# Optimization experiments

Measured on AMD Instinct MI355X. Metric: run time of the kernel, lower is better.

## Reference

```python
import jax, jax.numpy as jnp
import numpy as np

H, L, N = 512, 4096, 64

def make_dplr_hippo(n):
    # HiPPO-LegS -> NPLR -> DPLR diagonalization (numpy, init-time only)
    p0 = np.sqrt(1 + 2 * np.arange(n))
    A = p0[:, None] * p0[None, :]
    A = -(np.tril(A) - np.diag(np.arange(n)))
    p = np.sqrt(np.arange(n) + 0.5)
    b = np.sqrt(2 * np.arange(n) + 1.0)
    S = A + p[:, None] * p[None, :]
    Lambda_re = np.full(n, np.diagonal(S).mean())
    Lambda_im, V = np.linalg.eigh(S * -1j)
    Pc = V.conj().T @ p
    Bc = V.conj().T @ b
    return Lambda_re, Lambda_im, Pc, Bc

def setup_inputs() -> dict:
    key = jax.random.key(0)
    k_u, k_c, k_s = jax.random.split(key, 3)
    lr, li, Pc, Bc = make_dplr_hippo(N)
    tile = lambda v: jnp.tile(jnp.asarray(v, jnp.float32)[None, :], (H, 1))
    dt_min, dt_max = 0.001, 0.1
    log_step = (jax.random.uniform(k_s, (H, 1), jnp.float32)
                * (np.log(dt_max) - np.log(dt_min)) + np.log(dt_min))
    return {
        "u": jax.random.normal(k_u, (H, L), jnp.float32),
        "Lambda_re": tile(lr), "Lambda_im": tile(li),
        "P_re": tile(Pc.real), "P_im": tile(Pc.imag),
        "B_re": tile(Bc.real), "B_im": tile(Bc.imag),
        "C": jax.random.normal(k_c, (H, N, 2), jnp.float32) * (0.5 ** 0.5),
        "D": jnp.ones((H, 1), jnp.float32),
        "log_step": log_step,
    }

def reference(u, Lambda_re, Lambda_im, P_re, P_im, B_re, B_im, C, D, log_step):
    # u: [H, L]; all params leading dim H (vmapped channels)
    Lam = jnp.minimum(Lambda_re, -1e-4) + 1j * Lambda_im      # [H, N]
    P = P_re + 1j * P_im                                       # [H, N]
    B = B_re + 1j * B_im                                       # [H, N]
    Cc = C[..., 0] + 1j * C[..., 1]                             # [H, N]
    step = jnp.exp(log_step)                                    # [H, 1]
    Lseq = u.shape[-1]
    Omega = jnp.exp(-2j * jnp.pi * (jnp.arange(Lseq) / Lseq)).astype(jnp.complex64)  # [L]
    g = (2.0 / step) * ((1.0 - Omega) / (1.0 + Omega))[None, :]  # [H, L]
    c = 2.0 / (1.0 + Omega)                                      # [L]
    denom = 1.0 / (g[:, :, None] - Lam[:, None, :])              # [H, L, N]
    cauchy = lambda v: jnp.einsum('hn,hln->hl', v, denom)
    k00 = cauchy(Cc.conj() * B)
    k01 = cauchy(Cc.conj() * P)
    k10 = cauchy(P.conj() * B)
    k11 = cauchy(P.conj() * P)
    atRoots = c[None, :] * (k00 - k01 * (1.0 / (1.0 + k11)) * k10)
    K = jnp.fft.ifft(atRoots, Lseq, axis=-1).real                # [H, L] conv kernel
    # causal convolution via zero-padded FFT (length 2L)
    ud = jnp.fft.rfft(u, n=2 * Lseq, axis=-1)
    Kd = jnp.fft.rfft(K, n=2 * Lseq, axis=-1)
    y = jnp.fft.irfft(ud * Kd, n=2 * Lseq, axis=-1)[..., :Lseq]
    return y + D * u
```

## Files before the change

### kernel.cpp

```cpp
#include <hip/hip_runtime.h>
#include <math.h>

#define NT 512

typedef float v2 __attribute__((ext_vector_type(2)));

__device__ __forceinline__ v2 vrot(v2 a){ return (v2){-a.y, a.x}; }
__device__ __forceinline__ v2 vconj(v2 a){ return (v2){a.x, -a.y}; }
__device__ __forceinline__ v2 vcmul(v2 a, v2 b){ return a.x*b + a.y*vrot(b); }
__device__ __forceinline__ v2 vcmulc(v2 a, v2 b){
    return a.x*(v2){b.x, -b.y} + a.y*(v2){b.y, b.x};
}
__device__ __forceinline__ v2 vfma1(float s, v2 v, v2 acc){
    return (v2){ __builtin_fmaf(s, v.x, acc.x), __builtin_fmaf(s, v.y, acc.y) };
}

__device__ __forceinline__ int SW(int e){ return e ^ (((e>>5) ^ (e>>9)) & 15); }

__device__ __forceinline__ int d8r4(int x){
    return ((x&7)<<9) | (((x>>3)&7)<<6) | (((x>>6)&7)<<3) | ((x>>9)&7);
}
__device__ __forceinline__ int rev3(int t){
    return ((t&7)<<6) | (t&56) | ((t>>6)&7);
}

__device__ __forceinline__ void load_row(const v2* twd, int rowIdx, v2 W[7]) {
    const float4* rp4 = (const float4*)(twd + rowIdx*8);
    float4 q0 = rp4[0], q1 = rp4[1], q2 = rp4[2], q3 = rp4[3];
    W[0]=(v2){q0.x,q0.y}; W[1]=(v2){q0.z,q0.w}; W[2]=(v2){q1.x,q1.y};
    W[3]=(v2){q1.z,q1.w}; W[4]=(v2){q2.x,q2.y}; W[5]=(v2){q2.z,q2.w};
    W[6]=(v2){q3.x,q3.y};
}

__device__ __forceinline__ void dft8_inv(v2 t[8], v2 y[8]) {
    const float RH = 0.70710678f;
    v2 p  = t[0]+t[4], m  = t[0]-t[4], q  = t[2]+t[6], r  = t[2]-t[6];
    v2 rr = vrot(r);
    v2 E0 = p+q, E2 = p-q, E1 = m+rr, E3 = m-rr;
    v2 p2 = t[1]+t[5], m2 = t[1]-t[5], q2 = t[3]+t[7], r2 = t[3]-t[7];
    v2 rr2 = vrot(r2);
    v2 O0 = p2+q2, O2 = p2-q2, O1 = m2+rr2, O3 = m2-rr2;
    v2 W1O = RH*(O1 + vrot(O1));
    v2 W2O = vrot(O2);
    v2 W3O = vrot(RH*(O3 + vrot(O3)));
    y[0] = E0 + O0;  y[4] = E0 - O0;
    y[1] = E1 + W1O; y[5] = E1 - W1O;
    y[2] = E2 + W2O; y[6] = E2 - W2O;
    y[3] = E3 + W3O; y[7] = E3 - W3O;
}

__device__ __forceinline__ void dft8_inv_lo4(v2 t[8], v2 y[4]) {
    const float RH = 0.70710678f;
    v2 p  = t[0]+t[4], m  = t[0]-t[4], q  = t[2]+t[6], r  = t[2]-t[6];
    v2 rr = vrot(r);
    v2 E0 = p+q, E2 = p-q, E1 = m+rr, E3 = m-rr;
    v2 p2 = t[1]+t[5], m2 = t[1]-t[5], q2 = t[3]+t[7], r2 = t[3]-t[7];
    v2 rr2 = vrot(r2);
    v2 O0 = p2+q2, O2 = p2-q2, O1 = m2+rr2, O3 = m2-rr2;
    v2 W1O = RH*(O1 + vrot(O1));
    v2 W2O = vrot(O2);
    v2 W3O = vrot(RH*(O3 + vrot(O3)));
    y[0] = E0 + O0;
    y[1] = E1 + W1O;
    y[2] = E2 + W2O;
    y[3] = E3 + W3O;
}

__device__ __forceinline__ void dft8_fwd(v2 t[8], v2 y[8]) {
    const float RH = 0.70710678f;
    v2 p  = t[0]+t[4], m  = t[0]-t[4], q  = t[2]+t[6], r  = t[2]-t[6];
    v2 rr = vrot(r);
    v2 E0 = p+q, E2 = p-q, E1 = m-rr, E3 = m+rr;
    v2 p2 = t[1]+t[5], m2 = t[1]-t[5], q2 = t[3]+t[7], r2 = t[3]-t[7];
    v2 rr2 = vrot(r2);
    v2 O0 = p2+q2, O2 = p2-q2, O1 = m2-rr2, O3 = m2+rr2;
    v2 W1O = RH*(O1 - vrot(O1));
    v2 W2O = (v2){O2.y, -O2.x};
    v2 W3O = (-RH)*(O3 + vrot(O3));
    y[0] = E0 + O0;  y[4] = E0 - O0;
    y[1] = E1 + W1O; y[5] = E1 - W1O;
    y[2] = E2 + W2O; y[6] = E2 - W2O;
    y[3] = E3 + W3O; y[7] = E3 - W3O;
}


template<int Q, bool BAR>
__device__ __forceinline__ void r8_dit_inv(v2* buf, int tid, const v2* twd) {
    int j = tid & (Q-1);
    v2 W[7];
    load_row(twd, (512/Q)*j, W);
    int base = 8*tid - 7*j;
    v2 t[8];
    #pragma unroll
    for (int k = 0; k < 8; ++k) t[k] = buf[SW(base + k*Q)];
    #pragma unroll
    for (int k = 0; k < 7; ++k) t[k+1] = vcmul(t[k+1], W[k]);
    v2 y[8];
    dft8_inv(t, y);
    #pragma unroll
    for (int m = 0; m < 8; ++m) buf[SW(base + m*Q)] = y[m];
    if (BAR) __syncthreads();
    else     __builtin_amdgcn_wave_barrier();
}

template<int Q, bool BAR>
__device__ __forceinline__ void r8_dif_fwd(v2* buf, int tid, const v2* twd) {
    int j = tid & (Q-1);
    int baseL = 8*tid - 7*j;
    v2 W[7];
    if (Q > 1) load_row(twd, (512/Q)*j, W);
    #pragma unroll 1
    for (int hh = 0; hh < 2; ++hh) {
        int base = baseL + (hh << 12);
        v2 t[8];
        #pragma unroll
        for (int k = 0; k < 8; ++k) t[k] = buf[SW(base + k*Q)];
        v2 y[8];
        dft8_fwd(t, y);
        if (Q > 1) {
            #pragma unroll
            for (int k = 0; k < 7; ++k) y[k+1] = vcmulc(y[k+1], W[k]);
        }
        #pragma unroll
        for (int m = 0; m < 8; ++m) buf[SW(base + m*Q)] = y[m];
    }
    if (BAR) __syncthreads();
    else     __builtin_amdgcn_wave_barrier();
}

__global__ void __launch_bounds__(64)
s4_prep(const float* __restrict__ Lre, const float* __restrict__ Lim,
        const float* __restrict__ Pre, const float* __restrict__ Pim,
        const float* __restrict__ Bre, const float* __restrict__ Bim,
        const float* __restrict__ Cin,
        float* __restrict__ ws8, float* __restrict__ ws1)
{
    int idx = blockIdx.x*64 + threadIdx.x;
    float lre = fminf(Lre[idx], -1e-4f);
    float lim = Lim[idx];
    float pr = Pre[idx], pi = Pim[idx];
    float br = Bre[idx], bi = Bim[idx];
    float cr = Cin[2*idx], ci = Cin[2*idx+1];
    v2 cc = (v2){cr, -ci};
    v2 w00 = vcmul(cc, (v2){br, bi});
    v2 w01 = vcmul(cc, (v2){pr, pi});
    v2 w10 = vcmul((v2){pr,-pi}, (v2){br, bi});
    float* o = ws8 + idx*8;
    o[0] = -lre;  o[1] = -lim;
    o[2] = w00.x; o[3] = w00.y;
    o[4] = w01.x; o[5] = w01.y;
    o[6] = w10.x; o[7] = w10.y;
    ws1[idx] = pr*pr + pi*pi;
}

__global__ void __launch_bounds__(NT)
s4_twprep(v2* __restrict__ twd)
{
    int j = threadIdx.x;
    const float fm = 6.2831853072f / 4096.0f;
    #pragma unroll
    for (int k = 0; k < 7; ++k) {
        float s, c; __sincosf(fm * (float)(j*(k+1)), &s, &c);
        twd[j*8 + k] = (v2){c, s};
    }
    twd[j*8 + 7] = (v2){1.0f, 0.0f};
}

__global__ void __launch_bounds__(NT)
s4_fused(const float* __restrict__ u,
         const float* __restrict__ Din, const float* __restrict__ logstep,
         const float* __restrict__ ws8, const float* __restrict__ ws1,
         const v2* __restrict__ twd,
         float* __restrict__ out)
{
    __shared__ v2 buf[8192];
    const int tid = threadIdx.x;
    const int h = blockIdx.x;

    const float step = expf(logstep[h]);
    const float tos  = 2.0f / step;
    const float hstep = 0.5f * step;
    const float* pp = ws8 + (h*64)*8;
    const float* pw = ws1 + h*64;

    v2 a4[4];
    #pragma unroll 1
    for (int hp = 0; hp < 2; ++hp) {
        float tv[4];
        v2 cf[4], k00[4], k01[4], k10[4], k11[4];
        const int lbase = hp*(4*NT);
        #pragma unroll
        for (int i = 0; i < 4; ++i) {
            int l = lbase + i*NT + tid;
            float ang = -6.2831855f * ((float)l * (1.0f/4096.0f));
            float sh, ch; __sincosf(0.5f*ang, &sh, &ch);
            float traw = -tos * sh * __builtin_amdgcn_rcpf(ch);
            float t = fminf(fmaxf(traw, -1e18f), 1e18f);
            tv[i] = t;
            cf[i] = (v2){1.0f, t*hstep};
            k00[i]=(v2)(0.0f); k01[i]=(v2)(0.0f); k10[i]=(v2)(0.0f); k11[i]=(v2)(0.0f);
        }
        #pragma unroll 4
        for (int n = 0; n < 64; ++n) {
            float nlre = pp[n*8+0], nlim = pp[n*8+1];
            v2 w00 = (v2){pp[n*8+2], pp[n*8+3]};
            v2 w01 = (v2){pp[n*8+4], pp[n*8+5]};
            v2 w10 = (v2){pp[n*8+6], pp[n*8+7]};
            float w11r = pw[n];
            float lre2 = nlre*nlre;
            #pragma unroll
            for (int i = 0; i < 4; ++i) {
                float s = tv[i] + nlim;
                float inv = __builtin_amdgcn_rcpf(__builtin_fmaf(s, s, lre2));
                v2 p = (v2){nlre, s} * inv;
                v2 cp = (v2){p.x, -p.y};
                v2 rp = (v2){p.y,  p.x};
                k00[i] = vfma1(w00.y, rp, vfma1(w00.x, cp, k00[i]));
                k01[i] = vfma1(w01.y, rp, vfma1(w01.x, cp, k01[i]));
                k10[i] = vfma1(w10.y, rp, vfma1(w10.x, cp, k10[i]));
                k11[i] = vfma1(w11r,  cp, k11[i]);
            }
        }
        #pragma unroll
        for (int i = 0; i < 4; ++i) {
            v2 opk = (v2){1.0f + k11[i].x, k11[i].y};
            float iv = __builtin_amdgcn_rcpf(opk.x*opk.x + opk.y*opk.y);
            v2 r11 = vconj(opk) * iv;
            v2 t  = vcmul(vcmul(k01[i], r11), k10[i]);
            v2 res = vcmul(cf[i], k00[i] - t);
            if (hp == 0) buf[SW(tid + 512*i)] = res;
            else         a4[i] = res;
        }
    }
    {
        v2 t[8];
        #pragma unroll
        for (int k = 0; k < 4; ++k) t[k] = buf[SW(tid + 512*k)];
        #pragma unroll
        for (int k = 0; k < 4; ++k) t[4+k] = a4[k];
        __syncthreads();
        v2 y[8];
        dft8_inv(t, y);
        int tb8 = 8*rev3(tid);
        #pragma unroll
        for (int m = 0; m < 8; ++m) buf[SW(tb8 + m)] = y[m];
    }
    __syncthreads();

    r8_dit_inv<8,  false>(buf, tid, twd);
    r8_dit_inv<64, true >(buf, tid, twd);

    {
        v2 W[7];
        load_row(twd, tid, W);
        v2 t[8];
        #pragma unroll
        for (int k = 0; k < 8; ++k) t[k] = buf[SW(tid + 512*k)];
        #pragma unroll
        for (int k = 0; k < 7; ++k) t[k+1] = vcmul(t[k+1], W[k]);
        v2 y[8];
        dft8_inv(t, y);
        float uval[8];
        const float* up = u + h*4096;
        #pragma unroll
        for (int m = 0; m < 8; ++m) uval[m] = up[tid + 512*m];
        float s2, c2; __sincosf(-6.2831853072f/8192.0f*(float)tid, &s2, &c2);
        v2 cur0 = (v2){c2, s2};
        const v2 C16n = (v2){0.92387953f, -0.38268343f};
        v2 zL[8], zU[8];
        {
            v2 cur = cur0;
            #pragma unroll
            for (int k = 0; k < 8; ++k) {
                zL[k] = (v2){uval[k], y[k].x * (1.0f/4096.0f)};
                zU[k] = vcmul(zL[k], cur);
                cur = vcmul(cur, C16n);
            }
        }
        v2 s[8];
        dft8_fwd(zL, s);
        #pragma unroll
        for (int m = 1; m < 8; ++m) s[m] = vcmulc(s[m], W[m-1]);
        #pragma unroll
        for (int m = 0; m < 8; ++m) buf[SW(tid + 512*m)] = s[m];
        dft8_fwd(zU, s);
        #pragma unroll
        for (int m = 1; m < 8; ++m) s[m] = vcmulc(s[m], W[m-1]);
        #pragma unroll
        for (int m = 0; m < 8; ++m) buf[SW(4096 + tid + 512*m)] = s[m];
    }
    __syncthreads();

    r8_dif_fwd<64, false>(buf, tid, twd);
    r8_dif_fwd<8,  false>(buf, tid, twd);
    r8_dif_fwd<1,  true >(buf, tid, twd);

    {
        float sb, cb; __sincosf(6.2831853072f/8192.0f*(float)tid, &sb, &cb);
        v2 cur = (v2){cb, sb};
        const v2 C16p = (v2){0.92387953f, 0.38268343f};
        v2 v[8];
        #pragma unroll 1
        for (int i = 0; i < 8; ++i) {
            int r  = i*NT + tid;
            int par = (r&1)<<12;
            int e1 = par + d8r4(r>>1);
            int e3 = e1 + 4;
            int k2c = 4096 - r;
            int e4 = ((k2c&1)<<12) + d8r4((k2c>>1)&4095);
            int e2 = (r == 0) ? 0 : (e4 + 4);
            v2 za = buf[SW(e1)];
            v2 zb = buf[SW(e2)];
            v2 zc = buf[SW(e3)];
            v2 zd = buf[SW(e4)];
            v2 U1 = 0.5f*(za + vconj(zb));
            v2 K1 = -0.5f*vrot(za - vconj(zb));
            v2 Yr = vcmul(U1, K1);
            v2 U2 = 0.5f*(zc + vconj(zd));
            v2 K2 = -0.5f*vrot(zc - vconj(zd));
            v2 Ys = vcmul(U2, K2);
            v[i] = (Yr + Ys) + vrot(vcmul(cur, Yr - Ys));
            cur = vcmul(cur, C16p);
        }
        __syncthreads();
        v2 y[8];
        dft8_inv(v, y);
        int tb8 = 8*rev3(tid);
        #pragma unroll
        for (int m = 0; m < 8; ++m) buf[SW(tb8 + m)] = y[m];
    }
    __syncthreads();

    r8_dit_inv<8,  false>(buf, tid, twd);
    r8_dit_inv<64, true >(buf, tid, twd);

    {
        v2 W[7];
        load_row(twd, tid, W);
        v2 t[8];
        #pragma unroll
        for (int k = 0; k < 8; ++k) t[k] = buf[SW(tid + 512*k)];
        #pragma unroll
        for (int k = 0; k < 7; ++k) t[k+1] = vcmul(t[k+1], W[k]);
        v2 y[4];
        dft8_inv_lo4(t, y);
        const float Dh = Din[h];
        const float sc = 1.0f / 8192.0f;
        const v2* u2 = (const v2*)(u + h*4096);
        v2*     out2 = (v2*)(out + h*4096);
        #pragma unroll
        for (int m = 0; m < 4; ++m) {
            int n = tid + 512*m;
            out2[n] = sc*y[m] + Dh*u2[n];
        }
    }
}

extern "C" void kernel_launch(void* const* d_in, const int* in_sizes, int n_in,
                              void* d_out, int out_size, void* d_ws, size_t ws_size,
                              hipStream_t stream)
{
    const float* u       = (const float*)d_in[0];
    const float* Lre     = (const float*)d_in[1];
    const float* Lim     = (const float*)d_in[2];
    const float* Pre     = (const float*)d_in[3];
    const float* Pim     = (const float*)d_in[4];
    const float* Bre     = (const float*)d_in[5];
    const float* Bim     = (const float*)d_in[6];
    const float* Cin     = (const float*)d_in[7];
    const float* Din     = (const float*)d_in[8];
    const float* logstep = (const float*)d_in[9];
    float* out = (float*)d_out;
    const int H = in_sizes[8];

    float* ws8 = (float*)d_ws;
    float* ws1 = ws8 + (size_t)H*64*8;
    v2*    twd = (v2*)(ws1 + (size_t)H*64);

    hipLaunchKernelGGL(s4_prep, dim3(H), dim3(64), 0, stream,
                       Lre, Lim, Pre, Pim, Bre, Bim, Cin, ws8, ws1);
    hipLaunchKernelGGL(s4_twprep, dim3(1), dim3(NT), 0, stream, twd);
    hipLaunchKernelGGL(s4_fused, dim3(H), dim3(NT), 0, stream,
                       u, Din, logstep, ws8, ws1, twd, out);
}
```

Before: 156.5 us.

## Merge twiddle prep into prep kernel, bound occupancy, pack Cauchy denominators

The twiddle-table kernel is folded into the parameter-prep kernel as an extra trailing block, so one launch is removed. The fused kernel gains a launch_bounds minimum-blocks hint of 4, which pushes the compiler to cap register use and may cause spills. The Cauchy inner loop now computes its shifted denominators as packed two-wide vectors to encourage packed FP32 instructions.

```diff
diff --git a/kernel.cpp b/kernel.cpp
--- a/kernel.cpp
+++ b/kernel.cpp
@@ -133,9 +133,25 @@
         const float* __restrict__ Pre, const float* __restrict__ Pim,
         const float* __restrict__ Bre, const float* __restrict__ Bim,
         const float* __restrict__ Cin,
-        float* __restrict__ ws8, float* __restrict__ ws1)
+        float* __restrict__ ws8, float* __restrict__ ws1,
+        v2* __restrict__ twd)
 {
-    int idx = blockIdx.x*64 + threadIdx.x;
+    int b = blockIdx.x;
+    if (b == (int)gridDim.x - 1) {
+        const float fm = 6.2831853072f / 4096.0f;
+        #pragma unroll
+        for (int r = 0; r < 8; ++r) {
+            int j = r*64 + (int)threadIdx.x;
+            #pragma unroll
+            for (int k = 0; k < 7; ++k) {
+                float s, c; __sincosf(fm * (float)(j*(k+1)), &s, &c);
+                twd[j*8 + k] = (v2){c, s};
+            }
+            twd[j*8 + 7] = (v2){1.0f, 0.0f};
+        }
+        return;
+    }
+    int idx = b*64 + threadIdx.x;
     float lre = fminf(Lre[idx], -1e-4f);
     float lim = Lim[idx];
     float pr = Pre[idx], pi = Pim[idx];
@@ -153,20 +169,7 @@
     ws1[idx] = pr*pr + pi*pi;
 }
 
-__global__ void __launch_bounds__(NT)
-s4_twprep(v2* __restrict__ twd)
-{
-    int j = threadIdx.x;
-    const float fm = 6.2831853072f / 4096.0f;
-    #pragma unroll
-    for (int k = 0; k < 7; ++k) {
-        float s, c; __sincosf(fm * (float)(j*(k+1)), &s, &c);
-        twd[j*8 + k] = (v2){c, s};
-    }
-    twd[j*8 + 7] = (v2){1.0f, 0.0f};
-}
-
-__global__ void __launch_bounds__(NT)
+__global__ void __launch_bounds__(NT, 4)
 s4_fused(const float* __restrict__ u,
          const float* __restrict__ Din, const float* __restrict__ logstep,
          const float* __restrict__ ws8, const float* __restrict__ ws1,
@@ -200,6 +203,8 @@
             cf[i] = (v2){1.0f, t*hstep};
             k00[i]=(v2)(0.0f); k01[i]=(v2)(0.0f); k10[i]=(v2)(0.0f); k11[i]=(v2)(0.0f);
         }
+        const v2 tvA = (v2){tv[0], tv[1]};
+        const v2 tvB = (v2){tv[2], tv[3]};
         #pragma unroll 4
         for (int n = 0; n < 64; ++n) {
             float nlre = pp[n*8+0], nlim = pp[n*8+1];
@@ -208,11 +213,20 @@
             v2 w10 = (v2){pp[n*8+6], pp[n*8+7]};
             float w11r = pw[n];
             float lre2 = nlre*nlre;
+            v2 sA = tvA + (v2){nlim, nlim};
+            v2 sB = tvB + (v2){nlim, nlim};
+            v2 dA = (v2){ __builtin_fmaf(sA.x, sA.x, lre2),
+                          __builtin_fmaf(sA.y, sA.y, lre2) };
+            v2 dB = (v2){ __builtin_fmaf(sB.x, sB.x, lre2),
+                          __builtin_fmaf(sB.y, sB.y, lre2) };
+            float sv[4]   = { sA.x, sA.y, sB.x, sB.y };
+            float invv[4] = { __builtin_amdgcn_rcpf(dA.x),
+                              __builtin_amdgcn_rcpf(dA.y),
+                              __builtin_amdgcn_rcpf(dB.x),
+                              __builtin_amdgcn_rcpf(dB.y) };
             #pragma unroll
             for (int i = 0; i < 4; ++i) {
-                float s = tv[i] + nlim;
-                float inv = __builtin_amdgcn_rcpf(__builtin_fmaf(s, s, lre2));
-                v2 p = (v2){nlre, s} * inv;
+                v2 p = (v2){nlre, sv[i]} * invv[i];
                 v2 cp = (v2){p.x, -p.y};
                 v2 rp = (v2){p.y,  p.x};
                 k00[i] = vfma1(w00.y, rp, vfma1(w00.x, cp, k00[i]));
@@ -377,9 +391,8 @@
     float* ws1 = ws8 + (size_t)H*64*8;
     v2*    twd = (v2*)(ws1 + (size_t)H*64);
 
-    hipLaunchKernelGGL(s4_prep, dim3(H), dim3(64), 0, stream,
-                       Lre, Lim, Pre, Pim, Bre, Bim, Cin, ws8, ws1);
-    hipLaunchKernelGGL(s4_twprep, dim3(1), dim3(NT), 0, stream, twd);
+    hipLaunchKernelGGL(s4_prep, dim3(H + 1), dim3(64), 0, stream,
+                       Lre, Lim, Pre, Pim, Bre, Bim, Cin, ws8, ws1, twd);
     hipLaunchKernelGGL(s4_fused, dim3(H), dim3(NT), 0, stream,
                        u, Din, logstep, ws8, ws1, twd, out);
 }
```

Result: no change. 157.0 us (+0.3%).
